# Kernel optimization log

Measured on AMD Instinct MI355X. Metric: run time of the kernel, lower is better.

The kernel has to match this reference:

```python
import jax, jax.numpy as jnp
import numpy as np

N = 50000      # nodes per graph
E = 800000     # directed edges per graph
D_IN, C1, C2, C3, K = 96, 64, 32, 16, 16  # K = tensor_neurons (Linear(16,16) forces 16)


def setup_inputs() -> dict:
    key = jax.random.key(0)
    ks = jax.random.split(key, 18)
    def w(k, shape, scale=0.1):
        return (jax.random.normal(k, shape, jnp.float32) * scale)
    return {
        "features_1": jax.random.normal(ks[0], (N, D_IN), jnp.float32),
        "features_2": jax.random.normal(ks[1], (N, D_IN), jnp.float32),
        "edges_1": jax.random.randint(ks[2], (2, E), 0, N),
        "edges_2": jax.random.randint(ks[3], (2, E), 0, N),
        # GCN layer params (PyG GCNConv: X @ W then normalized aggregation, then + b)
        "W1": w(ks[4], (D_IN, C1)), "b1": jnp.zeros((C1,), jnp.float32),
        "W2": w(ks[5], (C1, C2)),  "b2": jnp.zeros((C2,), jnp.float32),
        "W3": w(ks[6], (C2, C3)),  "b3": jnp.zeros((C3,), jnp.float32),
        # Attention pooling weight matrix [C3, C3]
        "Wa": w(ks[7], (C3, C3)),
        # Tensor network: bilinear tensor [C3, C3, K], block [K, 2*C3], bias [K]
        "Wt": w(ks[8], (C3, C3, K)),
        "Wb": w(ks[9], (K, 2 * C3)),
        "bt": w(ks[10], (K,)),
        # fully_connected_first Linear(16,16) and scoring Linear(16,1)
        "Wfc": w(ks[11], (K, 16)), "bfc": jnp.zeros((16,), jnp.float32),
        "Wsc": w(ks[12], (16, 1)), "bsc": jnp.zeros((1,), jnp.float32),
    }


def gcn_conv(x, src, dst, W, b):
    # PyG GCNConv with self-loops: D^-1/2 (A+I) D^-1/2 (X W) + b
    h = x @ W                                   # [N, C]
    ones = jnp.ones(src.shape[0], h.dtype)
    deg = jax.ops.segment_sum(ones, dst, num_segments=N) + 1.0   # in-degree + self loop
    dinv = jax.lax.rsqrt(deg)                   # [N]
    coef = dinv[src] * dinv[dst]                # [E]
    agg = jax.ops.segment_sum(h[src] * coef[:, None], dst, num_segments=N)
    return agg + h * (dinv * dinv)[:, None] + b  # self-loop term has norm dinv_i^2


def encode(x, edges, W1, b1, W2, b2, W3, b3):
    src, dst = edges[0], edges[1]
    x = jax.nn.relu(gcn_conv(x, src, dst, W1, b1))  # dropout is a no-op in eval mode
    x = jax.nn.relu(gcn_conv(x, src, dst, W2, b2))
    return gcn_conv(x, src, dst, W3, b3)


def attention_pool(x, Wa):
    # SimGNN AttentionModule: c = tanh(mean(x Wa)); s = sigmoid(x c); rep = x^T s
    c = jnp.tanh(jnp.mean(x @ Wa, axis=0))      # [C3]
    s = jax.nn.sigmoid(x @ c)                   # [N]
    return x.T @ s                              # [C3]


def reference(features_1, features_2, edges_1, edges_2,
              W1, b1, W2, b2, W3, b3, Wa, Wt, Wb, bt, Wfc, bfc, Wsc, bsc):
    h1 = encode(features_1, edges_1, W1, b1, W2, b2, W3, b3)
    h2 = encode(features_2, edges_2, W1, b1, W2, b2, W3, b3)
    e1 = attention_pool(h1, Wa)                 # [C3]
    e2 = attention_pool(h2, Wa)                 # [C3]
    # Tensor network scoring
    bilinear = jnp.einsum('i,ijk,j->k', e1, Wt, e2)        # [K]
    block = Wb @ jnp.concatenate([e1, e2])                 # [K]
    scores = jax.nn.relu(bilinear + block + bt)            # [K]
    scores = jnp.tanh(scores @ Wfc + bfc)                  # [16]
    score = jax.nn.sigmoid(scores @ Wsc + bsc)             # [1]
    return score
```

## Files before the change

### kernel.cpp

```cpp
#include <hip/hip_runtime.h>
#include <hip/hip_bf16.h>

#define TPB 256
#define SH 6
#define BW 64

typedef unsigned short u16;
typedef __attribute__((ext_vector_type(8))) __bf16 bf16x8;
typedef __attribute__((ext_vector_type(4))) float f32x4;

__device__ __forceinline__ u16 f_to_bf(float f) {
    unsigned u = __float_as_uint(f);
    return (u16)((u + 0x7fff + ((u >> 16) & 1)) >> 16);
}
__device__ __forceinline__ float4 bf4_to_f4(ushort4 v) {
    float4 r;
    r.x = __uint_as_float((unsigned)v.x << 16);
    r.y = __uint_as_float((unsigned)v.y << 16);
    r.z = __uint_as_float((unsigned)v.z << 16);
    r.w = __uint_as_float((unsigned)v.w << 16);
    return r;
}


__global__ void bucket_count_kernel(const int* __restrict__ dst0, const int* __restrict__ dst1,
                                    int E, int* __restrict__ bcnt, int nbuk) {
    const int* dst = blockIdx.y ? dst1 : dst0;
    int* bc = bcnt + blockIdx.y * 1024;
    __shared__ int hist[1024];
    for (int t = threadIdx.x; t < 1024; t += TPB) hist[t] = 0;
    __syncthreads();
    int base = blockIdx.x * 8192;
    int end = min(base + 8192, E);
    for (int e = base + (int)threadIdx.x; e < end; e += TPB)
        atomicAdd(&hist[dst[e] >> SH], 1);
    __syncthreads();
    for (int t = threadIdx.x; t < nbuk; t += TPB) {
        int h = hist[t];
        if (h) atomicAdd(&bc[t], h);
    }
}

__global__ void bucket_scan_kernel(const int* __restrict__ bcnt, int nbuk,
                                   int* __restrict__ boff, int* __restrict__ bcur) {
    int g = blockIdx.x;
    const int* bc = bcnt + g * 1024;
    int* bo = boff + g * 1024;
    int* bu = bcur + g * 1024;
    __shared__ int s[1024];
    int t = threadIdx.x;
    int v = (t < nbuk) ? bc[t] : 0;
    s[t] = v;
    __syncthreads();
    for (int st = 1; st < 1024; st <<= 1) {
        int u = (t >= st) ? s[t - st] : 0;
        __syncthreads();
        s[t] += u;
        __syncthreads();
    }
    if (t < nbuk) { int e = s[t] - v; bo[t] = e; bu[t] = e; }
}

__global__ void bucket_scatter_kernel(const int* __restrict__ e0, const int* __restrict__ e1,
                                      int E, int* __restrict__ bcur,
                                      int* __restrict__ ebuf0, int* __restrict__ ebuf1, int nbuk) {
    int g = blockIdx.y;
    const int* src = g ? e1 : e0;
    const int* dst = src + E;
    int* ebuf = g ? ebuf1 : ebuf0;
    int* bu = bcur + g * 1024;
    __shared__ int hist[1024];
    for (int t = threadIdx.x; t < 1024; t += TPB) hist[t] = 0;
    __syncthreads();
    int base = blockIdx.x * 4096;
    int pk[16], bk[16], rk[16];
#pragma unroll
    for (int k = 0; k < 16; k++) {
        int e = base + k * TPB + (int)threadIdx.x;
        bk[k] = -1;
        if (e < E) {
            int s = src[e], d = dst[e];
            int b = d >> SH;
            bk[k] = b;
            pk[k] = (s << SH) | (d & (BW - 1));
            rk[k] = atomicAdd(&hist[b], 1);
        }
    }
    __syncthreads();
    for (int t = threadIdx.x; t < nbuk; t += TPB) {
        int h = hist[t];
        hist[t] = h ? atomicAdd(&bu[t], h) : 0;
    }
    __syncthreads();
#pragma unroll
    for (int k = 0; k < 16; k++)
        if (bk[k] >= 0) ebuf[hist[bk[k]] + rk[k]] = pk[k];
}

__global__ void bucket_csr_kernel(const int* __restrict__ ebuf0, const int* __restrict__ ebuf1,
                                  const int* __restrict__ boff, const int* __restrict__ bcnt,
                                  int n, int E,
                                  int* __restrict__ off0, int* __restrict__ off1,
                                  float* __restrict__ dinv0, float* __restrict__ dinv1,
                                  int* __restrict__ col0, int* __restrict__ col1) {
    int g = blockIdx.y;
    int b = blockIdx.x;
    const int* ebuf = g ? ebuf1 : ebuf0;
    int* off = g ? off1 : off0;
    float* dinv = g ? dinv1 : dinv0;
    int* col = g ? col1 : col0;
    __shared__ int h[BW], nb[BW], nrank[BW];
    int tid = threadIdx.x;
    if (tid < BW) h[tid] = 0;
    __syncthreads();
    int s = boff[g * 1024 + b], e = s + bcnt[g * 1024 + b];
    for (int i = s + tid; i < e; i += TPB)
        atomicAdd(&h[ebuf[i] & (BW - 1)], 1);
    __syncthreads();
    if (tid < BW) {
        int v = h[tid];
        int x = v;
        for (int d = 1; d < BW; d <<= 1) {
            int u = __shfl_up(x, d, 64);
            if (tid >= d) x += u;
        }
        int base = s + x - v;
        nb[tid] = base;
        nrank[tid] = 0;
        int node = b * BW + tid;
        if (node < n) {
            off[node] = base;
            dinv[node] = rsqrtf((float)v + 1.0f);
        }
        if (node == 0) off[n] = E;
    }
    __syncthreads();
    for (int i = s + tid; i < e; i += TPB) {
        int p = ebuf[i];
        int lo = p & (BW - 1);
        int r = atomicAdd(&nrank[lo], 1);
        col[nb[lo] + r] = p >> SH;
    }
}


template <int CIN, int COUT>
__global__ void matmul_kernel(const float* __restrict__ X0, const float* __restrict__ X1,
                              const float* __restrict__ W,
                              const float* __restrict__ dinv0, const float* __restrict__ dinv1,
                              u16* __restrict__ Y0, u16* __restrict__ Y1, int n) {
    constexpr int CINP = CIN + 8;
    constexpr int NT = COUT / 16;
    constexpr int KT = CIN / 32;
    __shared__ u16 Xs[64 * CINP];
    __shared__ u16 Wt[COUT * CINP];

    int g = blockIdx.y;
    const float* X = g ? X1 : X0;
    const float* dinv = g ? dinv1 : dinv0;
    u16* Y = g ? Y1 : Y0;
    int nb0 = blockIdx.x * 64;

    for (int i = threadIdx.x; i < 64 * (CIN / 4); i += TPB) {
        int nn = i / (CIN / 4), kc = i % (CIN / 4);
        float4 v = make_float4(0.f, 0.f, 0.f, 0.f);
        if (nb0 + nn < n) v = *(const float4*)&X[(size_t)(nb0 + nn) * CIN + 4 * kc];
        ushort4 b;
        b.x = f_to_bf(v.x); b.y = f_to_bf(v.y); b.z = f_to_bf(v.z); b.w = f_to_bf(v.w);
        *(ushort4*)&Xs[nn * CINP + 4 * kc] = b;
    }
    for (int i = threadIdx.x; i < CIN * (COUT / 4); i += TPB) {
        int k = i / (COUT / 4), nc4 = i % (COUT / 4);
        float4 v = *(const float4*)&W[(size_t)k * COUT + 4 * nc4];
        Wt[(4 * nc4 + 0) * CINP + k] = f_to_bf(v.x);
        Wt[(4 * nc4 + 1) * CINP + k] = f_to_bf(v.y);
        Wt[(4 * nc4 + 2) * CINP + k] = f_to_bf(v.z);
        Wt[(4 * nc4 + 3) * CINP + k] = f_to_bf(v.w);
    }
    __syncthreads();

    int lane = threadIdx.x & 63;
    int w = threadIdx.x >> 6;
    int m = lane & 15;
    int quad = lane >> 4;

    f32x4 acc[NT];
#pragma unroll
    for (int t = 0; t < NT; t++) acc[t] = (f32x4){0.f, 0.f, 0.f, 0.f};

#pragma unroll
    for (int kt = 0; kt < KT; kt++) {
        int k0 = kt * 32 + quad * 8;
        bf16x8 a = *(const bf16x8*)&Xs[(w * 16 + m) * CINP + k0];
#pragma unroll
        for (int t = 0; t < NT; t++) {
            bf16x8 b = *(const bf16x8*)&Wt[(t * 16 + m) * CINP + k0];
            acc[t] = __builtin_amdgcn_mfma_f32_16x16x32_bf16(a, b, acc[t], 0, 0, 0);
        }
    }

#pragma unroll
    for (int r = 0; r < 4; r++) {
        int node = nb0 + w * 16 + quad * 4 + r;
        if (node < n) {
            float d = dinv[node];
#pragma unroll
            for (int t = 0; t < NT; t++)
                Y[(size_t)node * COUT + t * 16 + m] = f_to_bf(acc[t][r] * d);
        }
    }
}


__device__ __forceinline__ void facc(float4& a, float4 v) {
    a.x += v.x; a.y += v.y; a.z += v.z; a.w += v.w;
}

template <int C>
__device__ __forceinline__ float4 gather_sum(const u16* __restrict__ HW,
                                             const int* __restrict__ col,
                                             int c0, int ps, int pe) {
    float4 a0 = make_float4(0.f, 0.f, 0.f, 0.f);
    float4 a1 = a0, a2 = a0, a3 = a0;
    int p = ps;
    for (; p + 4 <= pe; p += 4) {
        int j0 = col[p], j1 = col[p + 1], j2 = col[p + 2], j3 = col[p + 3];
        facc(a0, bf4_to_f4(*(const ushort4*)&HW[(size_t)j0 * C + c0]));
        facc(a1, bf4_to_f4(*(const ushort4*)&HW[(size_t)j1 * C + c0]));
        facc(a2, bf4_to_f4(*(const ushort4*)&HW[(size_t)j2 * C + c0]));
        facc(a3, bf4_to_f4(*(const ushort4*)&HW[(size_t)j3 * C + c0]));
    }
    for (; p < pe; p++) {
        int j = col[p];
        facc(a0, bf4_to_f4(*(const ushort4*)&HW[(size_t)j * C + c0]));
    }
    facc(a0, a1); facc(a2, a3); facc(a0, a2);
    return a0;
}

__device__ __forceinline__ float4 shfl_xor4(float4 v, int mask, int width) {
    v.x = __shfl_xor(v.x, mask, width);
    v.y = __shfl_xor(v.y, mask, width);
    v.z = __shfl_xor(v.z, mask, width);
    v.w = __shfl_xor(v.w, mask, width);
    return v;
}

template <int C, int SPLIT, bool RELU>
__global__ void agg_kernel(const u16* __restrict__ HW0, const u16* __restrict__ HW1,
                           const int* __restrict__ off0, const int* __restrict__ off1,
                           const int* __restrict__ col0, const int* __restrict__ col1,
                           const float* __restrict__ dinv0, const float* __restrict__ dinv1,
                           const float* __restrict__ bias,
                           float* __restrict__ out0, float* __restrict__ out1, int n) {
    int g = blockIdx.y;
    const u16* HW = g ? HW1 : HW0;
    const int* off = g ? off1 : off0;
    const int* col = g ? col1 : col0;
    const float* dinv = g ? dinv1 : dinv0;
    float* outp = g ? out1 : out0;
    constexpr int CH = C / 4;
    constexpr int TPN = CH * SPLIT;
    int tid = blockIdx.x * blockDim.x + threadIdx.x;
    int node = tid / TPN;
    if (node >= n) return;
    int part = tid % TPN;
    int sp = part / CH;
    int c0 = (part % CH) * 4;
    int s = off[node], e = off[node + 1];
    int len = e - s;
    int chunk = (len + SPLIT - 1) / SPLIT;
    int ps = s + sp * chunk;
    int pe = min(ps + chunk, e);
    float4 r = gather_sum<C>(HW, col, c0, ps, pe);
#pragma unroll
    for (int m = CH; m < TPN; m <<= 1) facc(r, shfl_xor4(r, m, TPN));
    if (sp == 0) {
        float di = dinv[node];
        float4 self = bf4_to_f4(*(const ushort4*)&HW[(size_t)node * C + c0]);
        float4 b4 = *(const float4*)&bias[c0];
        float4 o;
        o.x = di * (r.x + self.x) + b4.x;
        o.y = di * (r.y + self.y) + b4.y;
        o.z = di * (r.z + self.z) + b4.z;
        o.w = di * (r.w + self.w) + b4.w;
        if (RELU) {
            o.x = fmaxf(o.x, 0.f); o.y = fmaxf(o.y, 0.f);
            o.z = fmaxf(o.z, 0.f); o.w = fmaxf(o.w, 0.f);
        }
        *(float4*)&outp[(size_t)node * C + c0] = o;
    }
}


__global__ void colsum_kernel(const float* __restrict__ H0, const float* __restrict__ H1,
                              int n, float* __restrict__ colsum) {
    int g = blockIdx.y;
    const float* H = g ? H1 : H0;
    int c = threadIdx.x % 16;
    int w = (blockIdx.x * blockDim.x + threadIdx.x) / 16;
    int stride = (gridDim.x * blockDim.x) / 16;
    float acc = 0.f;
    for (int node = w; node < n; node += stride) acc += H[(size_t)node * 16 + c];
    __shared__ float sdata[TPB];
    sdata[threadIdx.x] = acc;
    __syncthreads();
    if (threadIdx.x < 16) {
        float s = 0.f;
        for (int t = threadIdx.x; t < TPB; t += 16) s += sdata[t];
        atomicAdd(&colsum[g * 16 + threadIdx.x], s);
    }
}

__global__ void cvec_kernel(const float* __restrict__ colsum, const float* __restrict__ Wa,
                            float n_inv, float* __restrict__ cvec) {
    int g = blockIdx.x;
    int j = threadIdx.x;
    if (j < 16) {
        const float* cs = colsum + g * 16;
        float acc = 0.f;
        for (int i = 0; i < 16; i++) acc += (cs[i] * n_inv) * Wa[i * 16 + j];
        cvec[g * 16 + j] = tanhf(acc);
    }
}

__global__ void pool_kernel(const float* __restrict__ H0, const float* __restrict__ H1, int n,
                            const float* __restrict__ cvec, float* __restrict__ rep) {
    int g = blockIdx.y;
    const float* H = g ? H1 : H0;
    int c = threadIdx.x % 16;
    float cv = cvec[g * 16 + c];
    int w = (blockIdx.x * blockDim.x + threadIdx.x) / 16;
    int stride = (gridDim.x * blockDim.x) / 16;
    float acc = 0.f;
    for (int node = w; node < n; node += stride) {
        float x = H[(size_t)node * 16 + c];
        float p = x * cv;
        p += __shfl_xor(p, 1, 16);
        p += __shfl_xor(p, 2, 16);
        p += __shfl_xor(p, 4, 16);
        p += __shfl_xor(p, 8, 16);
        float s = 1.f / (1.f + __expf(-p));
        acc += s * x;
    }
    __shared__ float sdata[TPB];
    sdata[threadIdx.x] = acc;
    __syncthreads();
    if (threadIdx.x < 16) {
        float s = 0.f;
        for (int t = threadIdx.x; t < TPB; t += 16) s += sdata[t];
        atomicAdd(&rep[g * 16 + threadIdx.x], s);
    }
}


__global__ void final_kernel(const float* __restrict__ rep,
                             const float* __restrict__ Wt, const float* __restrict__ Wb,
                             const float* __restrict__ bt, const float* __restrict__ Wfc,
                             const float* __restrict__ bfc, const float* __restrict__ Wsc,
                             const float* __restrict__ bsc, float* __restrict__ out) {
    const float* e1 = rep;
    const float* e2 = rep + 16;
    __shared__ float scores[16], tvec[16], se1[16], se2[16];
    int t = threadIdx.x;
    if (t < 16) { se1[t] = e1[t]; se2[t] = e2[t]; }
    __syncthreads();
    if (t < 16) {
        float bil = 0.f;
        for (int i = 0; i < 16; i++) {
            float a = se1[i];
            for (int j = 0; j < 16; j++) bil += a * se2[j] * Wt[(i * 16 + j) * 16 + t];
        }
        float blk = 0.f;
        for (int m = 0; m < 16; m++)
            blk += Wb[t * 32 + m] * se1[m] + Wb[t * 32 + 16 + m] * se2[m];
        scores[t] = fmaxf(bil + blk + bt[t], 0.f);
    }
    __syncthreads();
    if (t < 16) {
        float acc = bfc[t];
        for (int k = 0; k < 16; k++) acc += scores[k] * Wfc[k * 16 + t];
        tvec[t] = tanhf(acc);
    }
    __syncthreads();
    if (t == 0) {
        float acc = bsc[0];
        for (int j = 0; j < 16; j++) acc += tvec[j] * Wsc[j];
        out[0] = 1.f / (1.f + __expf(-acc));
    }
}


extern "C" void kernel_launch(void* const* d_in, const int* in_sizes, int n_in,
                              void* d_out, int out_size, void* d_ws, size_t ws_size,
                              hipStream_t stream) {
    const float* X1 = (const float*)d_in[0];
    const float* X2 = (const float*)d_in[1];
    const int* edges1 = (const int*)d_in[2];
    const int* edges2 = (const int*)d_in[3];
    const float* W1 = (const float*)d_in[4];
    const float* b1 = (const float*)d_in[5];
    const float* W2 = (const float*)d_in[6];
    const float* b2 = (const float*)d_in[7];
    const float* W3 = (const float*)d_in[8];
    const float* b3 = (const float*)d_in[9];
    const float* Wa = (const float*)d_in[10];
    const float* Wt = (const float*)d_in[11];
    const float* Wb = (const float*)d_in[12];
    const float* bt = (const float*)d_in[13];
    const float* Wfc = (const float*)d_in[14];
    const float* bfc = (const float*)d_in[15];
    const float* Wsc = (const float*)d_in[16];
    const float* bsc = (const float*)d_in[17];
    float* out = (float*)d_out;

    const int N = in_sizes[0] / 96;
    const int E = in_sizes[2] / 2;
    const int NBUK = (N + BW - 1) / BW;

    char* ws = (char*)d_ws;
    size_t o = 0;
    auto alloc = [&](size_t bytes) {
        void* p = ws + o;
        o += (bytes + 255) & ~(size_t)255;
        return p;
    };
    int* bcnt = (int*)alloc((size_t)2 * 1024 * 4);
    float* small = (float*)alloc(96 * 4);
    float* colsum = small;
    float* cvec = small + 32;
    float* rep = small + 64;
    int* boff = (int*)alloc((size_t)2 * 1024 * 4);
    int* bcur = (int*)alloc((size_t)2 * 1024 * 4);
    int* off0 = (int*)alloc((size_t)(N + 1) * 4);
    int* off1 = (int*)alloc((size_t)(N + 1) * 4);
    int* col0 = (int*)alloc((size_t)E * 4);
    int* col1 = (int*)alloc((size_t)E * 4);
    float* dinv0 = (float*)alloc((size_t)N * 4);
    float* dinv1 = (float*)alloc((size_t)N * 4);
    int* ebuf0 = (int*)alloc((size_t)E * 4);
    int* ebuf1 = (int*)alloc((size_t)E * 4);
    u16* hwb0 = (u16*)alloc((size_t)N * 64 * 2);
    u16* hwb1 = (u16*)alloc((size_t)N * 64 * 2);
    float* bufB0 = (float*)alloc((size_t)N * 64 * 4);
    float* bufB1 = (float*)alloc((size_t)N * 64 * 4);

    const int gB1 = (E + 8191) / 8192;
    const int gB2 = (E + 4095) / 4096;
    const int g16 = ((size_t)N * 16 + TPB - 1) / TPB;
    const int gMM = (N + 63) / 64;

    hipMemsetAsync(bcnt, 0, (size_t)2 * 1024 * 4 + 96 * 4, stream);

    bucket_count_kernel<<<dim3(gB1, 2), TPB, 0, stream>>>(edges1 + E, edges2 + E, E, bcnt, NBUK);
    bucket_scan_kernel<<<2, 1024, 0, stream>>>(bcnt, NBUK, boff, bcur);
    bucket_scatter_kernel<<<dim3(gB2, 2), TPB, 0, stream>>>(edges1, edges2, E, bcur, ebuf0, ebuf1, NBUK);
    bucket_csr_kernel<<<dim3(NBUK, 2), TPB, 0, stream>>>(ebuf0, ebuf1, boff, bcnt, N, E,
                                                         off0, off1, dinv0, dinv1, col0, col1);

    matmul_kernel<96, 64><<<dim3(gMM, 2), TPB, 0, stream>>>(X1, X2, W1, dinv0, dinv1, hwb0, hwb1, N);
    agg_kernel<64, 1, true><<<dim3(g16, 2), TPB, 0, stream>>>(
        hwb0, hwb1, off0, off1, col0, col1, dinv0, dinv1, b1, bufB0, bufB1, N);
    matmul_kernel<64, 32><<<dim3(gMM, 2), TPB, 0, stream>>>(bufB0, bufB1, W2, dinv0, dinv1, hwb0, hwb1, N);
    agg_kernel<32, 2, true><<<dim3(g16, 2), TPB, 0, stream>>>(
        hwb0, hwb1, off0, off1, col0, col1, dinv0, dinv1, b2, bufB0, bufB1, N);
    matmul_kernel<32, 16><<<dim3(gMM, 2), TPB, 0, stream>>>(bufB0, bufB1, W3, dinv0, dinv1, hwb0, hwb1, N);
    agg_kernel<16, 4, false><<<dim3(g16, 2), TPB, 0, stream>>>(
        hwb0, hwb1, off0, off1, col0, col1, dinv0, dinv1, b3, bufB0, bufB1, N);

    colsum_kernel<<<dim3(64, 2), TPB, 0, stream>>>(bufB0, bufB1, N, colsum);
    cvec_kernel<<<2, 64, 0, stream>>>(colsum, Wa, 1.0f / (float)N, cvec);
    pool_kernel<<<dim3(64, 2), TPB, 0, stream>>>(bufB0, bufB1, N, cvec, rep);

    final_kernel<<<1, 64, 0, stream>>>(rep, Wt, Wb, bt, Wfc, bfc, Wsc, bsc, out);
}
```

Before: 293.0 us.

## Fuse column-sum into last aggregation and cvec into pool kernel

The final GCN aggregation kernel now also reduces its outputs per block into partial column sums, which replaces the separate colsum pass over the layer-3 output. The pool kernel reduces those partials and computes the attention context vector itself, removing the cvec kernel. Atomics on small accumulators are replaced by per-block partial buffers that later kernels reduce, so part of the memset goes away. This removes two launches and one full read of the node features, at the cost of redundant partial reductions in every pool block.

```diff
diff --git a/kernel.cpp b/kernel.cpp
--- a/kernel.cpp
+++ b/kernel.cpp
@@ -20,6 +20,38 @@
     r.z = __uint_as_float((unsigned)v.z << 16);
     r.w = __uint_as_float((unsigned)v.w << 16);
     return r;
+}
+__device__ __forceinline__ void facc(float4& a, float4 v) {
+    a.x += v.x; a.y += v.y; a.z += v.z; a.w += v.w;
+}
+__device__ __forceinline__ float4 shfl_xor4(float4 v, int mask, int width) {
+    v.x = __shfl_xor(v.x, mask, width);
+    v.y = __shfl_xor(v.y, mask, width);
+    v.z = __shfl_xor(v.z, mask, width);
+    v.w = __shfl_xor(v.w, mask, width);
+    return v;
+}
+
+template <int C>
+__device__ __forceinline__ float4 gather_sum(const u16* __restrict__ HW,
+                                             const int* __restrict__ col,
+                                             int c0, int ps, int pe) {
+    float4 a0 = make_float4(0.f, 0.f, 0.f, 0.f);
+    float4 a1 = a0, a2 = a0, a3 = a0;
+    int p = ps;
+    for (; p + 4 <= pe; p += 4) {
+        int j0 = col[p], j1 = col[p + 1], j2 = col[p + 2], j3 = col[p + 3];
+        facc(a0, bf4_to_f4(*(const ushort4*)&HW[(size_t)j0 * C + c0]));
+        facc(a1, bf4_to_f4(*(const ushort4*)&HW[(size_t)j1 * C + c0]));
+        facc(a2, bf4_to_f4(*(const ushort4*)&HW[(size_t)j2 * C + c0]));
+        facc(a3, bf4_to_f4(*(const ushort4*)&HW[(size_t)j3 * C + c0]));
+    }
+    for (; p < pe; p++) {
+        int j = col[p];
+        facc(a0, bf4_to_f4(*(const ushort4*)&HW[(size_t)j * C + c0]));
+    }
+    facc(a0, a1); facc(a2, a3); facc(a0, a2);
+    return a0;
 }
 
 
@@ -187,7 +219,6 @@
     f32x4 acc[NT];
 #pragma unroll
     for (int t = 0; t < NT; t++) acc[t] = (f32x4){0.f, 0.f, 0.f, 0.f};
-
 #pragma unroll
     for (int kt = 0; kt < KT; kt++) {
         int k0 = kt * 32 + quad * 8;
@@ -198,7 +229,6 @@
             acc[t] = __builtin_amdgcn_mfma_f32_16x16x32_bf16(a, b, acc[t], 0, 0, 0);
         }
     }
-
 #pragma unroll
     for (int r = 0; r < 4; r++) {
         int node = nb0 + w * 16 + quad * 4 + r;
@@ -211,40 +241,6 @@
     }
 }
 
-
-__device__ __forceinline__ void facc(float4& a, float4 v) {
-    a.x += v.x; a.y += v.y; a.z += v.z; a.w += v.w;
-}
-
-template <int C>
-__device__ __forceinline__ float4 gather_sum(const u16* __restrict__ HW,
-                                             const int* __restrict__ col,
-                                             int c0, int ps, int pe) {
-    float4 a0 = make_float4(0.f, 0.f, 0.f, 0.f);
-    float4 a1 = a0, a2 = a0, a3 = a0;
-    int p = ps;
-    for (; p + 4 <= pe; p += 4) {
-        int j0 = col[p], j1 = col[p + 1], j2 = col[p + 2], j3 = col[p + 3];
-        facc(a0, bf4_to_f4(*(const ushort4*)&HW[(size_t)j0 * C + c0]));
-        facc(a1, bf4_to_f4(*(const ushort4*)&HW[(size_t)j1 * C + c0]));
-        facc(a2, bf4_to_f4(*(const ushort4*)&HW[(size_t)j2 * C + c0]));
-        facc(a3, bf4_to_f4(*(const ushort4*)&HW[(size_t)j3 * C + c0]));
-    }
-    for (; p < pe; p++) {
-        int j = col[p];
-        facc(a0, bf4_to_f4(*(const ushort4*)&HW[(size_t)j * C + c0]));
-    }
-    facc(a0, a1); facc(a2, a3); facc(a0, a2);
-    return a0;
-}
-
-__device__ __forceinline__ float4 shfl_xor4(float4 v, int mask, int width) {
-    v.x = __shfl_xor(v.x, mask, width);
-    v.y = __shfl_xor(v.y, mask, width);
-    v.z = __shfl_xor(v.z, mask, width);
-    v.w = __shfl_xor(v.w, mask, width);
-    return v;
-}
 
 template <int C, int SPLIT, bool RELU>
 __global__ void agg_kernel(const u16* __restrict__ HW0, const u16* __restrict__ HW1,
@@ -292,44 +288,98 @@
     }
 }
 
-
-__global__ void colsum_kernel(const float* __restrict__ H0, const float* __restrict__ H1,
-                              int n, float* __restrict__ colsum) {
+__global__ void agg16_kernel(const u16* __restrict__ HW0, const u16* __restrict__ HW1,
+                             const int* __restrict__ off0, const int* __restrict__ off1,
+                             const int* __restrict__ col0, const int* __restrict__ col1,
+                             const float* __restrict__ dinv0, const float* __restrict__ dinv1,
+                             const float* __restrict__ bias,
+                             float* __restrict__ out0, float* __restrict__ out1,
+                             float* __restrict__ pcol, int n) {
+    int g = blockIdx.y;
+    const u16* HW = g ? HW1 : HW0;
+    const int* off = g ? off1 : off0;
+    const int* col = g ? col1 : col0;
+    const float* dinv = g ? dinv1 : dinv0;
+    float* outp = g ? out1 : out0;
+    int tid = blockIdx.x * blockDim.x + threadIdx.x;
+    int node = tid / 16;
+    int part = tid % 16;
+    int sp = part / 4;
+    int c0 = (part % 4) * 4;
+    float4 o = make_float4(0.f, 0.f, 0.f, 0.f);
+    if (node < n) {
+        int s = off[node], e = off[node + 1];
+        int len = e - s;
+        int chunk = (len + 3) / 4;
+        int ps = s + sp * chunk;
+        int pe = min(ps + chunk, e);
+        float4 r = gather_sum<16>(HW, col, c0, ps, pe);
+        facc(r, shfl_xor4(r, 4, 16));
+        facc(r, shfl_xor4(r, 8, 16));
+        if (sp == 0) {
+            float di = dinv[node];
+            float4 self = bf4_to_f4(*(const ushort4*)&HW[(size_t)node * 16 + c0]);
+            float4 b4 = *(const float4*)&bias[c0];
+            o.x = di * (r.x + self.x) + b4.x;
+            o.y = di * (r.y + self.y) + b4.y;
+            o.z = di * (r.z + self.z) + b4.z;
+            o.w = di * (r.w + self.w) + b4.w;
+            *(float4*)&outp[(size_t)node * 16 + c0] = o;
+        }
+    }
+    __shared__ float4 sd[TPB];
+    sd[threadIdx.x] = (node < n && sp == 0) ? o : make_float4(0.f, 0.f, 0.f, 0.f);
+    __syncthreads();
+    if (threadIdx.x < 64) {
+        float4 a = sd[threadIdx.x];
+        facc(a, sd[threadIdx.x + 64]);
+        facc(a, sd[threadIdx.x + 128]);
+        facc(a, sd[threadIdx.x + 192]);
+        sd[threadIdx.x] = a;
+    }
+    __syncthreads();
+    if (threadIdx.x < 16) {
+        float4 a = sd[threadIdx.x];
+        facc(a, sd[threadIdx.x + 16]);
+        facc(a, sd[threadIdx.x + 32]);
+        facc(a, sd[threadIdx.x + 48]);
+        sd[threadIdx.x] = a;
+    }
+    __syncthreads();
+    if (threadIdx.x < 4)
+        *(float4*)&pcol[((size_t)g * gridDim.x + blockIdx.x) * 16 + threadIdx.x * 4] = sd[threadIdx.x];
+}
+
+
+__global__ void pool_kernel(const float* __restrict__ H0, const float* __restrict__ H1, int n,
+                            const float* __restrict__ pcol, int nb16, float n_inv,
+                            const float* __restrict__ Wa, float* __restrict__ ppool) {
     int g = blockIdx.y;
     const float* H = g ? H1 : H0;
-    int c = threadIdx.x % 16;
-    int w = (blockIdx.x * blockDim.x + threadIdx.x) / 16;
-    int stride = (gridDim.x * blockDim.x) / 16;
-    float acc = 0.f;
-    for (int node = w; node < n; node += stride) acc += H[(size_t)node * 16 + c];
     __shared__ float sdata[TPB];
-    sdata[threadIdx.x] = acc;
-    __syncthreads();
-    if (threadIdx.x < 16) {
+    __shared__ float cs[16];
+    __shared__ float cvecS[16];
+    int c = threadIdx.x & 15;
+    {
+        int chunk = threadIdx.x >> 4;
         float s = 0.f;
-        for (int t = threadIdx.x; t < TPB; t += 16) s += sdata[t];
-        atomicAdd(&colsum[g * 16 + threadIdx.x], s);
-    }
-}
-
-__global__ void cvec_kernel(const float* __restrict__ colsum, const float* __restrict__ Wa,
-                            float n_inv, float* __restrict__ cvec) {
-    int g = blockIdx.x;
-    int j = threadIdx.x;
-    if (j < 16) {
-        const float* cs = colsum + g * 16;
-        float acc = 0.f;
-        for (int i = 0; i < 16; i++) acc += (cs[i] * n_inv) * Wa[i * 16 + j];
-        cvec[g * 16 + j] = tanhf(acc);
-    }
-}
-
-__global__ void pool_kernel(const float* __restrict__ H0, const float* __restrict__ H1, int n,
-                            const float* __restrict__ cvec, float* __restrict__ rep) {
-    int g = blockIdx.y;
-    const float* H = g ? H1 : H0;
-    int c = threadIdx.x % 16;
-    float cv = cvec[g * 16 + c];
+        for (int b = chunk; b < nb16; b += 16) s += pcol[((size_t)g * nb16 + b) * 16 + c];
+        sdata[threadIdx.x] = s;
+        __syncthreads();
+        if (threadIdx.x < 16) {
+            float t = 0.f;
+            for (int k = threadIdx.x; k < TPB; k += 16) t += sdata[k];
+            cs[threadIdx.x] = t * n_inv;
+        }
+        __syncthreads();
+        if (threadIdx.x < 16) {
+            float acc = 0.f;
+            for (int i = 0; i < 16; i++) acc += cs[i] * Wa[i * 16 + threadIdx.x];
+            cvecS[threadIdx.x] = tanhf(acc);
+        }
+        __syncthreads();
+    }
+    float cv = cvecS[c];
     int w = (blockIdx.x * blockDim.x + threadIdx.x) / 16;
     int stride = (gridDim.x * blockDim.x) / 16;
     float acc = 0.f;
@@ -343,37 +393,40 @@
         float s = 1.f / (1.f + __expf(-p));
         acc += s * x;
     }
-    __shared__ float sdata[TPB];
+    __syncthreads();
     sdata[threadIdx.x] = acc;
     __syncthreads();
     if (threadIdx.x < 16) {
         float s = 0.f;
         for (int t = threadIdx.x; t < TPB; t += 16) s += sdata[t];
-        atomicAdd(&rep[g * 16 + threadIdx.x], s);
-    }
-}
-
-
-__global__ void final_kernel(const float* __restrict__ rep,
+        ppool[((size_t)g * gridDim.x + blockIdx.x) * 16 + threadIdx.x] = s;
+    }
+}
+
+
+__global__ void final_kernel(const float* __restrict__ ppool, int nbp,
                              const float* __restrict__ Wt, const float* __restrict__ Wb,
                              const float* __restrict__ bt, const float* __restrict__ Wfc,
                              const float* __restrict__ bfc, const float* __restrict__ Wsc,
                              const float* __restrict__ bsc, float* __restrict__ out) {
-    const float* e1 = rep;
-    const float* e2 = rep + 16;
-    __shared__ float scores[16], tvec[16], se1[16], se2[16];
+    __shared__ float rep[32], scores[16], tvec[16];
     int t = threadIdx.x;
-    if (t < 16) { se1[t] = e1[t]; se2[t] = e2[t]; }
+    if (t < 32) {
+        int g = t >> 4, c = t & 15;
+        float s = 0.f;
+        for (int b = 0; b < nbp; b++) s += ppool[((size_t)g * nbp + b) * 16 + c];
+        rep[t] = s;
+    }
     __syncthreads();
     if (t < 16) {
         float bil = 0.f;
         for (int i = 0; i < 16; i++) {
-            float a = se1[i];
-            for (int j = 0; j < 16; j++) bil += a * se2[j] * Wt[(i * 16 + j) * 16 + t];
+            float a = rep[i];
+            for (int j = 0; j < 16; j++) bil += a * rep[16 + j] * Wt[(i * 16 + j) * 16 + t];
         }
         float blk = 0.f;
         for (int m = 0; m < 16; m++)
-            blk += Wb[t * 32 + m] * se1[m] + Wb[t * 32 + 16 + m] * se2[m];
+            blk += Wb[t * 32 + m] * rep[m] + Wb[t * 32 + 16 + m] * rep[16 + m];
         scores[t] = fmaxf(bil + blk + bt[t], 0.f);
     }
     __syncthreads();
@@ -426,10 +479,6 @@
         return p;
     };
     int* bcnt = (int*)alloc((size_t)2 * 1024 * 4);
-    float* small = (float*)alloc(96 * 4);
-    float* colsum = small;
-    float* cvec = small + 32;
-    float* rep = small + 64;
     int* boff = (int*)alloc((size_t)2 * 1024 * 4);
     int* bcur = (int*)alloc((size_t)2 * 1024 * 4);
     int* off0 = (int*)alloc((size_t)(N + 1) * 4);
@@ -449,8 +498,12 @@
     const int gB2 = (E + 4095) / 4096;
     const int g16 = ((size_t)N * 16 + TPB - 1) / TPB;
     const int gMM = (N + 63) / 64;
-
-    hipMemsetAsync(bcnt, 0, (size_t)2 * 1024 * 4 + 96 * 4, stream);
+    const int gPool = 64;
+
+    float* pcol = (float*)alloc((size_t)2 * g16 * 16 * 4);
+    float* ppool = (float*)alloc((size_t)2 * gPool * 16 * 4);
+
+    hipMemsetAsync(bcnt, 0, (size_t)2 * 1024 * 4, stream);
 
     bucket_count_kernel<<<dim3(gB1, 2), TPB, 0, stream>>>(edges1 + E, edges2 + E, E, bcnt, NBUK);
     bucket_scan_kernel<<<2, 1024, 0, stream>>>(bcnt, NBUK, boff, bcur);
@@ -465,12 +518,10 @@
     agg_kernel<32, 2, true><<<dim3(g16, 2), TPB, 0, stream>>>(
         hwb0, hwb1, off0, off1, col0, col1, dinv0, dinv1, b2, bufB0, bufB1, N);
     matmul_kernel<32, 16><<<dim3(gMM, 2), TPB, 0, stream>>>(bufB0, bufB1, W3, dinv0, dinv1, hwb0, hwb1, N);
-    agg_kernel<16, 4, false><<<dim3(g16, 2), TPB, 0, stream>>>(
-        hwb0, hwb1, off0, off1, col0, col1, dinv0, dinv1, b3, bufB0, bufB1, N);
-
-    colsum_kernel<<<dim3(64, 2), TPB, 0, stream>>>(bufB0, bufB1, N, colsum);
-    cvec_kernel<<<2, 64, 0, stream>>>(colsum, Wa, 1.0f / (float)N, cvec);
-    pool_kernel<<<dim3(64, 2), TPB, 0, stream>>>(bufB0, bufB1, N, cvec, rep);
-
-    final_kernel<<<1, 64, 0, stream>>>(rep, Wt, Wb, bt, Wfc, bfc, Wsc, bsc, out);
-}
+    agg16_kernel<<<dim3(g16, 2), TPB, 0, stream>>>(
+        hwb0, hwb1, off0, off1, col0, col1, dinv0, dinv1, b3, bufB0, bufB1, pcol, N);
+
+    pool_kernel<<<dim3(gPool, 2), TPB, 0, stream>>>(bufB0, bufB1, N, pcol, g16,
+                                                    1.0f / (float)N, Wa, ppool);
+    final_kernel<<<1, 256, 0, stream>>>(ppool, gPool, Wt, Wb, bt, Wfc, bfc, Wsc, bsc, out);
+}
```

Measured after the change: 341.4 us. +16.5%, slower.
